# Optimization experiments

Measured on AMD Instinct MI355X. Metric: run time of the kernel, lower is better.

## Reference

```python
import jax, jax.numpy as jnp
import numpy as np

B, J, D, W, H, EH, L = 128, 8192, 32, 4, 128, 256, 32
TEMP = 1.0


def _ln(x, g, b, eps=1e-5):
    mu = jnp.mean(x, axis=-1, keepdims=True)
    var = jnp.var(x, axis=-1, keepdims=True)
    return (x - mu) * jax.lax.rsqrt(var + eps) * g + b


def setup_inputs() -> dict:
    key = jax.random.key(0)
    ks = jax.random.split(key, 12)

    def lin(k, fi, fo):
        k1, k2 = jax.random.split(k)
        s = 1.0 / np.sqrt(fi)
        return (jax.random.uniform(k1, (fi, fo), minval=-s, maxval=s, dtype=jnp.float32),
                jax.random.uniform(k2, (fo,), minval=-s, maxval=s, dtype=jnp.float32))

    h_w1, h_b1 = lin(ks[0], 1 + D, H)
    h_w2, h_b2 = lin(ks[1], H, D)
    g_w1, g_b1 = lin(ks[2], D, D // 2)
    g_w2, g_b2 = lin(ks[3], D // 2, W)
    c_w, c_b = lin(ks[4], W * D, D)
    e_w1, e_b1 = lin(ks[5], D, EH)
    e_w2, e_b2 = lin(ks[6], EH, 2 * L)
    return {
        'x': jax.random.normal(ks[7], (B, J), dtype=jnp.float32),
        'mask': jax.random.randint(ks[8], (B, J), 0, 2, dtype=jnp.int32),
        'fe': jax.random.normal(ks[9], (J, D), dtype=jnp.float32),
        'h_w1': h_w1, 'h_b1': h_b1,
        'h_ln1_w': jnp.ones((H,), jnp.float32), 'h_ln1_b': jnp.zeros((H,), jnp.float32),
        'h_w2': h_w2, 'h_b2': h_b2,
        'h_ln2_w': jnp.ones((D,), jnp.float32), 'h_ln2_b': jnp.zeros((D,), jnp.float32),
        'g_w1': g_w1, 'g_b1': g_b1, 'g_w2': g_w2, 'g_b2': g_b2,
        'c_w': c_w, 'c_b': c_b,
        'c_ln_w': jnp.ones((D,), jnp.float32), 'c_ln_b': jnp.zeros((D,), jnp.float32),
        'e_w1': e_w1, 'e_b1': e_b1,
        'e_ln1_w': jnp.ones((EH,), jnp.float32), 'e_ln1_b': jnp.zeros((EH,), jnp.float32),
        'e_w2': e_w2, 'e_b2': e_b2,
        'e_ln2_w': jnp.ones((2 * L,), jnp.float32), 'e_ln2_b': jnp.zeros((2 * L,), jnp.float32),
    }


def _forward(x, mask, fe, h_w1, h_b1, h_ln1_w, h_ln1_b, h_w2, h_b2, h_ln2_w, h_ln2_b,
             g_w1, g_b1, g_w2, g_b2, c_w, c_b, c_ln_w, c_ln_b,
             e_w1, e_b1, e_ln1_w, e_ln1_b, e_w2, e_b2, e_ln2_w, e_ln2_b):
    relu = jax.nn.relu
    # h_in = concat([x, F]) @ h_w1 split into scalar column + shared embedding part
    # (fe @ h_w1[1:]) is [J,H], shared across cells -> avoids materializing [B,J,1+D]
    pre = x[..., None] * h_w1[0][None, None, :] + (fe @ h_w1[1:])[None] + h_b1  # [B,J,H]
    h1 = relu(_ln(pre, h_ln1_w, h_ln1_b))
    h_out = relu(_ln(h1 @ h_w2 + h_b2, h_ln2_w, h_ln2_b))  # [B,J,D]
    raw_gates = relu(h_out @ g_w1 + g_b1) @ g_w2 + g_b2  # [B,J,W]
    logits = jnp.clip(raw_gates * TEMP, -10.0, 10.0)
    logits = jnp.where(mask[..., None] > 0, logits, -1e9)  # masked gather -> -inf fill
    weights = jax.nn.softmax(logits, axis=1)  # softmax over observed junctions
    head_sums = jnp.einsum('bjw,bjd->bwd', weights, h_out)  # [B,W,D]
    comb = relu(_ln(head_sums.reshape(head_sums.shape[0], -1) @ c_w + c_b, c_ln_w, c_ln_b))
    comb = jnp.where((jnp.sum(mask, axis=1) > 0)[:, None], comb, 0.0)  # zero cells -> zeros
    h = relu(_ln(comb @ e_w1 + e_b1, e_ln1_w, e_ln1_b))
    o = relu(_ln(h @ e_w2 + e_b2, e_ln2_w, e_ln2_b))
    mu, logvar = jnp.split(o, 2, axis=-1)
    return mu, logvar


def reference(x, mask, fe, h_w1, h_b1, h_ln1_w, h_ln1_b, h_w2, h_b2, h_ln2_w, h_ln2_b,
              g_w1, g_b1, g_w2, g_b2, c_w, c_b, c_ln_w, c_ln_b,
              e_w1, e_b1, e_ln1_w, e_ln1_b, e_w2, e_b2, e_ln2_w, e_ln2_b):
    return _forward(x, mask, fe, h_w1, h_b1, h_ln1_w, h_ln1_b, h_w2, h_b2, h_ln2_w, h_ln2_b,
                    g_w1, g_b1, g_w2, g_b2, c_w, c_b, c_ln_w, c_ln_b,
                    e_w1, e_b1, e_ln1_w, e_ln1_b, e_w2, e_b2, e_ln2_w, e_ln2_b)
```

## Files before the change

kernel.cpp:

```cpp
#include <hip/hip_runtime.h>
#include <cstdint>

#define BDIM 128
#define JDIM 8192

typedef short s8x __attribute__((ext_vector_type(8)));
typedef float f4x __attribute__((ext_vector_type(4)));

__device__ __forceinline__ unsigned int rne16(float f) {
    unsigned int u = __float_as_uint(f);
    return (u + 0x7fffu + ((u >> 16) & 1u)) >> 16;
}
__device__ __forceinline__ unsigned int pkbf(float lo, float hi) {
    return rne16(lo) | (rne16(hi) << 16);
}
__device__ __forceinline__ float bf2f(unsigned int s) {
    return __uint_as_float(s << 16);
}

__global__ __launch_bounds__(128) void k_prep(
    const float* __restrict__ fe, const float* __restrict__ hw1,
    const float* __restrict__ hb1,
    unsigned short* __restrict__ feWb, float* __restrict__ aux,
    float* __restrict__ scal)
{
    const int j = blockIdx.x, h = threadIdx.x;
    float acc = hb1[h];
#pragma unroll
    for (int d = 0; d < 32; ++d)
        acc = fmaf(fe[j * 32 + d], hw1[(1 + d) * 128 + h], acc);
    feWb[(size_t)j * 128 + h] = (unsigned short)rne16(acc);

    const float w0h = hw1[h];
    float s1 = acc, sx = w0h * acc, s2 = acc * acc;
#pragma unroll
    for (int m = 1; m <= 32; m <<= 1) {
        s1 += __shfl_xor(s1, m); sx += __shfl_xor(sx, m); s2 += __shfl_xor(s2, m);
    }
    __shared__ float red[2][3];
    const int wv = threadIdx.x >> 6, ln = threadIdx.x & 63;
    if (ln == 0) { red[wv][0] = s1; red[wv][1] = sx; red[wv][2] = s2; }
    __syncthreads();
    if (threadIdx.x == 0) {
        aux[j * 4 + 0] = (red[0][0] + red[1][0]) * (1.f / 128.f);
        aux[j * 4 + 1] = (red[0][1] + red[1][1]) * (1.f / 128.f);
        aux[j * 4 + 2] = (red[0][2] + red[1][2]) * (1.f / 128.f);
    }
    if (j == 0) {
        float a = w0h, b = w0h * w0h;
#pragma unroll
        for (int m = 1; m <= 32; m <<= 1) { a += __shfl_xor(a, m); b += __shfl_xor(b, m); }
        __syncthreads();
        if (ln == 0) { red[wv][0] = a; red[wv][1] = b; }
        __syncthreads();
        if (threadIdx.x == 0) {
            scal[0] = (red[0][0] + red[1][0]) * (1.f / 128.f);
            scal[1] = (red[0][1] + red[1][1]) * (1.f / 128.f);
        }
    }
}

__global__ __launch_bounds__(256, 2) void k_main(
    const float* __restrict__ x, const int* __restrict__ mask,
    const unsigned short* __restrict__ feWb, const float* __restrict__ aux,
    const float* __restrict__ scal,
    const float* __restrict__ hw1, const float* __restrict__ ln1w,
    const float* __restrict__ ln1b,
    const float* __restrict__ hw2, const float* __restrict__ hb2,
    const float* __restrict__ ln2w, const float* __restrict__ ln2b,
    const float* __restrict__ gw1, const float* __restrict__ gb1,
    const float* __restrict__ gw2, const float* __restrict__ gb2,
    float* __restrict__ P, float* __restrict__ SEb)
{
    __shared__ float w0s[128], g1s[128], b1s[128];
    __shared__ float holds[8][576];
    __shared__ float hsL[2048];
    __shared__ float seL[64];

    const int tid = threadIdx.x, wv = tid >> 6, l = tid & 63;
    const int c = l & 15, g = l >> 4;
    const int bt = blockIdx.y, bx = blockIdx.x;
    const int b0 = bt * 16;

    if (tid < 128) { w0s[tid] = hw1[tid]; g1s[tid] = ln1w[tid]; b1s[tid] = ln1b[tid]; }
    __syncthreads();

    const float mw0 = scal[0], q0 = scal[1];

    s8x wf[2][4];
#pragma unroll
    for (int nt = 0; nt < 2; ++nt)
#pragma unroll
        for (int t = 0; t < 4; ++t) {
            const int kb = 32 * t + 8 * g, n = 16 * nt + c;
            uint4 u;
            u.x = pkbf(hw2[(kb + 0) * 32 + n], hw2[(kb + 1) * 32 + n]);
            u.y = pkbf(hw2[(kb + 2) * 32 + n], hw2[(kb + 3) * 32 + n]);
            u.z = pkbf(hw2[(kb + 4) * 32 + n], hw2[(kb + 5) * 32 + n]);
            u.w = pkbf(hw2[(kb + 6) * 32 + n], hw2[(kb + 7) * 32 + n]);
            wf[nt][t] = __builtin_bit_cast(s8x, u);
        }
    s8x g1f;
    {
        uint4 u;
        u.x = pkbf(gw1[(8 * g + 0) * 16 + c], gw1[(8 * g + 1) * 16 + c]);
        u.y = pkbf(gw1[(8 * g + 2) * 16 + c], gw1[(8 * g + 3) * 16 + c]);
        u.z = pkbf(gw1[(8 * g + 4) * 16 + c], gw1[(8 * g + 5) * 16 + c]);
        u.w = pkbf(gw1[(8 * g + 6) * 16 + c], gw1[(8 * g + 7) * 16 + c]);
        g1f = __builtin_bit_cast(s8x, u);
    }
    const float hb2a = hb2[c],      hb2b = hb2[16 + c];
    const float g2a  = ln2w[c],     g2b  = ln2w[16 + c];
    const float z2a  = ln2b[c],     z2b  = ln2b[16 + c];
    const float gb1c = gb1[c];
    float gw2c[4], gb2v[4];
#pragma unroll
    for (int w = 0; w < 4; ++w) { gw2c[w] = gw2[c * 4 + w]; gb2v[w] = gb2[w]; }

    const int j0 = (bx * 4 + wv) * 32;
    const float* xrow = x + (size_t)(b0 + c) * JDIM;
    const int*   mrow = mask + (size_t)(b0 + c) * JDIM;

    float hsacc[4][4][2];
    float seacc[4][4];
#pragma unroll
    for (int r = 0; r < 4; ++r)
#pragma unroll
        for (int w = 0; w < 4; ++w) {
            hsacc[r][w][0] = 0.f; hsacc[r][w][1] = 0.f; seacc[r][w] = 0.f;
        }

    for (int jj = 0; jj < 32; ++jj) {
        const int j = j0 + jj;
        const float xv = xrow[j];
        const int   mv = mrow[j];
        const float m1 = aux[j * 4 + 0], qx = aux[j * 4 + 1], q2 = aux[j * 4 + 2];
        const float mu = fmaf(xv, mw0, m1);
        const float e2 = fmaf(xv * xv, q0, fmaf(2.f * xv, qx, q2));
        const float rs = rsqrtf(e2 - mu * mu + 1e-5f);
        const float nms = -mu * rs;

        f4x ca = {0.f, 0.f, 0.f, 0.f}, cbv = {0.f, 0.f, 0.f, 0.f};
        const unsigned short* fj = feWb + (size_t)j * 128;
#pragma unroll
        for (int t = 0; t < 4; ++t) {
            const int kb = 32 * t + 8 * g;
            const uint4 fw = *(const uint4*)(fj + kb);
            const float pf0 = bf2f(fw.x & 0xffffu), pf1 = bf2f(fw.x >> 16);
            const float pf2 = bf2f(fw.y & 0xffffu), pf3 = bf2f(fw.y >> 16);
            const float pf4 = bf2f(fw.z & 0xffffu), pf5 = bf2f(fw.z >> 16);
            const float pf6 = bf2f(fw.w & 0xffffu), pf7 = bf2f(fw.w >> 16);
            const float4 wa = *(const float4*)&w0s[kb];
            const float4 wb = *(const float4*)&w0s[kb + 4];
            const float4 ga = *(const float4*)&g1s[kb];
            const float4 gbq = *(const float4*)&g1s[kb + 4];
            const float4 ba = *(const float4*)&b1s[kb];
            const float4 bb = *(const float4*)&b1s[kb + 4];
            const float h0 = fmaxf(fmaf(fmaf(fmaf(xv, wa.x, pf0), rs, nms), ga.x,  ba.x), 0.f);
            const float h1 = fmaxf(fmaf(fmaf(fmaf(xv, wa.y, pf1), rs, nms), ga.y,  ba.y), 0.f);
            const float h2 = fmaxf(fmaf(fmaf(fmaf(xv, wa.z, pf2), rs, nms), ga.z,  ba.z), 0.f);
            const float h3 = fmaxf(fmaf(fmaf(fmaf(xv, wa.w, pf3), rs, nms), ga.w,  ba.w), 0.f);
            const float h4 = fmaxf(fmaf(fmaf(fmaf(xv, wb.x, pf4), rs, nms), gbq.x, bb.x), 0.f);
            const float h5 = fmaxf(fmaf(fmaf(fmaf(xv, wb.y, pf5), rs, nms), gbq.y, bb.y), 0.f);
            const float h6 = fmaxf(fmaf(fmaf(fmaf(xv, wb.z, pf6), rs, nms), gbq.z, bb.z), 0.f);
            const float h7 = fmaxf(fmaf(fmaf(fmaf(xv, wb.w, pf7), rs, nms), gbq.w, bb.w), 0.f);
            uint4 u;
            u.x = pkbf(h0, h1); u.y = pkbf(h2, h3); u.z = pkbf(h4, h5); u.w = pkbf(h6, h7);
            const s8x af = __builtin_bit_cast(s8x, u);
            ca  = __builtin_amdgcn_mfma_f32_16x16x32_bf16(af, wf[0][t], ca,  0, 0, 0);
            cbv = __builtin_amdgcn_mfma_f32_16x16x32_bf16(af, wf[1][t], cbv, 0, 0, 0);
        }

        float v0[4], v1[4], sr[4], qr[4];
#pragma unroll
        for (int r = 0; r < 4; ++r) {
            v0[r] = ca[r] + hb2a;
            v1[r] = cbv[r] + hb2b;
            sr[r] = v0[r] + v1[r];
            qr[r] = v0[r] * v0[r] + v1[r] * v1[r];
        }
#pragma unroll
        for (int m = 1; m <= 8; m <<= 1)
#pragma unroll
            for (int r = 0; r < 4; ++r) {
                sr[r] += __shfl_xor(sr[r], m);
                qr[r] += __shfl_xor(qr[r], m);
            }
        float ho0[4], ho1[4];
#pragma unroll
        for (int r = 0; r < 4; ++r) {
            const float m2  = sr[r] * 0.03125f;
            const float rs2 = rsqrtf(fmaf(qr[r], 0.03125f, -m2 * m2) + 1e-5f);
            const float nm2 = -m2 * rs2;
            ho0[r] = fmaxf(fmaf(fmaf(v0[r], rs2, nm2), g2a, z2a), 0.f);
            ho1[r] = fmaxf(fmaf(fmaf(v1[r], rs2, nm2), g2b, z2b), 0.f);
        }

        float* hp = &holds[wv * 2 + (jj & 1)][0];
#pragma unroll
        for (int r = 0; r < 4; ++r) {
            hp[(4 * g + r) * 36 + c]      = ho0[r];
            hp[(4 * g + r) * 36 + 16 + c] = ho1[r];
        }
        asm volatile("s_waitcnt lgkmcnt(0)" ::: "memory");
        const float4 ra  = *(const float4*)&hp[c * 36 + 8 * g];
        const float4 rb2 = *(const float4*)&hp[c * 36 + 8 * g + 4];
        uint4 ua;
        ua.x = pkbf(ra.x, ra.y);  ua.y = pkbf(ra.z, ra.w);
        ua.z = pkbf(rb2.x, rb2.y); ua.w = pkbf(rb2.z, rb2.w);
        const s8x af2 = __builtin_bit_cast(s8x, ua);
        f4x gc = {0.f, 0.f, 0.f, 0.f};
        gc = __builtin_amdgcn_mfma_f32_16x16x32_bf16(af2, g1f, gc, 0, 0, 0);

        float pw[16];
#pragma unroll
        for (int r = 0; r < 4; ++r) {
            const float g1r = fmaxf(gc[r] + gb1c, 0.f);
#pragma unroll
            for (int w = 0; w < 4; ++w) pw[r * 4 + w] = g1r * gw2c[w];
        }
#pragma unroll
        for (int m = 1; m <= 8; m <<= 1)
#pragma unroll
            for (int i = 0; i < 16; ++i) pw[i] += __shfl_xor(pw[i], m);

        int mc[4];
#pragma unroll
        for (int r = 0; r < 4; ++r) mc[r] = __shfl(mv, 20 * g + r);

#pragma unroll
        for (int r = 0; r < 4; ++r)
#pragma unroll
            for (int w = 0; w < 4; ++w) {
                const float lg = fminf(fmaxf(pw[r * 4 + w] + gb2v[w], -10.f), 10.f);
                const float e  = (mc[r] > 0) ? __expf(lg - 10.f) : 0.f;
                seacc[r][w] += e;
                hsacc[r][w][0] = fmaf(e, ho0[r], hsacc[r][w][0]);
                hsacc[r][w][1] = fmaf(e, ho1[r], hsacc[r][w][1]);
            }
    }

    for (int ww = 0; ww < 4; ++ww) {
        __syncthreads();
        if (wv == ww) {
#pragma unroll
            for (int r = 0; r < 4; ++r)
#pragma unroll
                for (int w = 0; w < 4; ++w)
#pragma unroll
                    for (int nt = 0; nt < 2; ++nt) {
                        const int idx = ((4 * g + r) * 4 + w) * 32 + c + 16 * nt;
                        if (ww == 0) hsL[idx] = hsacc[r][w][nt];
                        else         hsL[idx] += hsacc[r][w][nt];
                    }
            if (c == 0) {
#pragma unroll
                for (int r = 0; r < 4; ++r)
#pragma unroll
                    for (int w = 0; w < 4; ++w) {
                        const int si = (4 * g + r) * 4 + w;
                        if (ww == 0) seL[si] = seacc[r][w];
                        else         seL[si] += seacc[r][w];
                    }
            }
        }
    }
    __syncthreads();
    const size_t base = ((size_t)bt * 64 + bx) * 2048;
    for (int i = tid; i < 2048; i += 256) P[base + i] = hsL[i];
    if (tid < 64) SEb[((size_t)bt * 64 + bx) * 64 + tid] = seL[tid];
}

__global__ __launch_bounds__(128) void k_tail(
    const float* __restrict__ P, const float* __restrict__ SEb,
    const float* __restrict__ cw, const float* __restrict__ cbv,
    const float* __restrict__ clnw, const float* __restrict__ clnb,
    const float* __restrict__ ew1, const float* __restrict__ eb1,
    const float* __restrict__ l1w, const float* __restrict__ l1b,
    const float* __restrict__ ew2, const float* __restrict__ eb2,
    const float* __restrict__ l2w, const float* __restrict__ l2b,
    float* __restrict__ out)
{
    const int b = blockIdx.x, t = threadIdx.x;
    const int bt = b >> 4, bi = b & 15;
    __shared__ float hsLs[128], combL[32], hL[256], seW[4], sred[64], red[4];

    const float* Pb = P + (size_t)bt * 64 * 2048 + bi * 128;
    float sacc = 0.f;
#pragma unroll 4
    for (int jc = 0; jc < 64; ++jc) sacc += Pb[(size_t)jc * 2048 + t];

    if (t < 64) {
        const int w = t & 3, sl = t >> 2;
        const float* Sb = SEb + (size_t)bt * 64 * 64 + bi * 4 + w;
        float sp = 0.f;
#pragma unroll
        for (int q = 0; q < 4; ++q) sp += Sb[(size_t)(sl * 4 + q) * 64];
        sred[t] = sp;
    }
    __syncthreads();
    if (t < 4) {
        float v = 0.f;
#pragma unroll
        for (int sl = 0; sl < 16; ++sl) v += sred[sl * 4 + t];
        seW[t] = v;
    }
    __syncthreads();
    const bool has = seW[0] > 0.f;
    hsLs[t] = has ? sacc / seW[t >> 5] : 0.f;
    __syncthreads();

    if (t < 32) {
        float cv = cbv[t];
#pragma unroll 4
        for (int f = 0; f < 128; ++f) cv = fmaf(hsLs[f], cw[f * 32 + t], cv);
        float s = cv, q = cv * cv;
#pragma unroll
        for (int m = 1; m <= 16; m <<= 1) { s += __shfl_xor(s, m); q += __shfl_xor(q, m); }
        const float mu = s * (1.f / 32.f);
        const float rsg = rsqrtf(fmaf(q, 1.f / 32.f, -mu * mu) + 1e-5f);
        const float v = fmaf(fmaf(cv, rsg, -mu * rsg), clnw[t], clnb[t]);
        combL[t] = has ? fmaxf(v, 0.f) : 0.f;
    }
    __syncthreads();

    float h0 = eb1[t], h1v = eb1[t + 128];
#pragma unroll 4
    for (int d = 0; d < 32; ++d) {
        const float cd = combL[d];
        h0  = fmaf(cd, ew1[d * 256 + t], h0);
        h1v = fmaf(cd, ew1[d * 256 + t + 128], h1v);
    }
    {
        float s = h0 + h1v, q = h0 * h0 + h1v * h1v;
#pragma unroll
        for (int m = 1; m <= 32; m <<= 1) { s += __shfl_xor(s, m); q += __shfl_xor(q, m); }
        const int wv = t >> 6, ln = t & 63;
        if (ln == 0) { red[wv * 2] = s; red[wv * 2 + 1] = q; }
    }
    __syncthreads();
    {
        const float S = red[0] + red[2], Q = red[1] + red[3];
        const float mu1 = S * (1.f / 256.f);
        const float rs1 = rsqrtf(fmaf(Q, 1.f / 256.f, -mu1 * mu1) + 1e-5f);
        hL[t]       = fmaxf(fmaf(fmaf(h0,  rs1, -mu1 * rs1), l1w[t],       l1b[t]),       0.f);
        hL[t + 128] = fmaxf(fmaf(fmaf(h1v, rs1, -mu1 * rs1), l1w[t + 128], l1b[t + 128]), 0.f);
    }
    __syncthreads();

    if (t < 64) {
        float ov = eb2[t];
#pragma unroll 4
        for (int m = 0; m < 256; ++m) ov = fmaf(hL[m], ew2[m * 64 + t], ov);
        float s = ov, q = ov * ov;
#pragma unroll
        for (int m = 1; m <= 32; m <<= 1) { s += __shfl_xor(s, m); q += __shfl_xor(q, m); }
        const float mu2 = s * (1.f / 64.f);
        const float rs2 = rsqrtf(fmaf(q, 1.f / 64.f, -mu2 * mu2) + 1e-5f);
        const float o = fmaxf(fmaf(fmaf(ov, rs2, -mu2 * rs2), l2w[t], l2b[t]), 0.f);
        if (t < 32) out[b * 32 + t] = o;
        else        out[4096 + b * 32 + (t - 32)] = o;
    }
}

extern "C" void kernel_launch(void* const* d_in, const int* in_sizes, int n_in,
                              void* d_out, int out_size, void* d_ws, size_t ws_size,
                              hipStream_t stream)
{
    (void)in_sizes; (void)n_in; (void)out_size; (void)ws_size;
    const float* x    = (const float*)d_in[0];
    const int*   mask = (const int*)d_in[1];
    const float* fe   = (const float*)d_in[2];
    const float* hw1  = (const float*)d_in[3];
    const float* hb1  = (const float*)d_in[4];
    const float* ln1w = (const float*)d_in[5];
    const float* ln1b = (const float*)d_in[6];
    const float* hw2  = (const float*)d_in[7];
    const float* hb2  = (const float*)d_in[8];
    const float* ln2w = (const float*)d_in[9];
    const float* ln2b = (const float*)d_in[10];
    const float* gw1  = (const float*)d_in[11];
    const float* gb1  = (const float*)d_in[12];
    const float* gw2  = (const float*)d_in[13];
    const float* gb2  = (const float*)d_in[14];
    const float* cw   = (const float*)d_in[15];
    const float* cbv  = (const float*)d_in[16];
    const float* clnw = (const float*)d_in[17];
    const float* clnb = (const float*)d_in[18];
    const float* ew1  = (const float*)d_in[19];
    const float* eb1  = (const float*)d_in[20];
    const float* l1w  = (const float*)d_in[21];
    const float* l1b  = (const float*)d_in[22];
    const float* ew2  = (const float*)d_in[23];
    const float* eb2  = (const float*)d_in[24];
    const float* l2w  = (const float*)d_in[25];
    const float* l2b  = (const float*)d_in[26];

    char* ws = (char*)d_ws;
    unsigned short* feWb = (unsigned short*)ws;
    float* aux  = (float*)(ws + (2u << 20));
    float* scal = (float*)(ws + (2u << 20) + (128u << 10));
    float* P    = (float*)(ws + (2u << 20) + (128u << 10) + 256u);
    float* SEb  = (float*)(ws + (2u << 20) + (128u << 10) + 256u + 8u * 64u * 2048u * 4u);

    hipLaunchKernelGGL(k_prep, dim3(JDIM), dim3(128), 0, stream,
                       fe, hw1, hb1, feWb, aux, scal);
    hipLaunchKernelGGL(k_main, dim3(64, 8), dim3(256), 0, stream,
                       x, mask, feWb, aux, scal,
                       hw1, ln1w, ln1b, hw2, hb2, ln2w, ln2b,
                       gw1, gb1, gw2, gb2, P, SEb);
    hipLaunchKernelGGL(k_tail, dim3(BDIM), dim3(128), 0, stream,
                       P, SEb, cw, cbv, clnw, clnb,
                       ew1, eb1, l1w, l1b, ew2, eb2, l2w, l2b,
                       (float*)d_out);
}
```

Before: 262.9 us.

## Double j-split blocks, use DPP reductions, ballot mask, and raise occupancy

Splits the junction dimension into twice as many blocks (when workspace allows), so the main kernel launches 1024 blocks instead of 512 and each wave handles 16 junctions. It raises the launch-bounds occupancy hint to 4 blocks per CU. It replaces the shfl_xor butterfly reductions across 16 lanes with DPP row operations, builds the mask bits with a ballot instead of per-row shuffles, and uses exp2 with one FMA and a single float4 load for the aux values. The tail kernel now reduces over the variable number of partial blocks, which costs more partial-sum traffic, and the higher occupancy target may force register spills.

New measurement: 284.7 us. 1.08x slower.

```diff
diff --git a/kernel.cpp b/kernel.cpp
--- a/kernel.cpp
+++ b/kernel.cpp
@@ -16,6 +16,19 @@
 }
 __device__ __forceinline__ float bf2f(unsigned int s) {
     return __uint_as_float(s << 16);
+}
+
+template <int CTRL>
+__device__ __forceinline__ float dppadd(float x) {
+    int y = __builtin_amdgcn_update_dpp(0, __builtin_bit_cast(int, x), CTRL, 0xF, 0xF, true);
+    return x + __builtin_bit_cast(float, y);
+}
+__device__ __forceinline__ float allred16(float x) {
+    x = dppadd<0xB1>(x);
+    x = dppadd<0x4E>(x);
+    x = dppadd<0x141>(x);
+    x = dppadd<0x140>(x);
+    return x;
 }
 
 __global__ __launch_bounds__(128) void k_prep(
@@ -60,7 +73,7 @@
     }
 }
 
-__global__ __launch_bounds__(256, 2) void k_main(
+__global__ __launch_bounds__(256, 4) void k_main(
     const float* __restrict__ x, const int* __restrict__ mask,
     const unsigned short* __restrict__ feWb, const float* __restrict__ aux,
     const float* __restrict__ scal,
@@ -70,14 +83,15 @@
     const float* __restrict__ ln2w, const float* __restrict__ ln2b,
     const float* __restrict__ gw1, const float* __restrict__ gb1,
     const float* __restrict__ gw2, const float* __restrict__ gb2,
-    float* __restrict__ P, float* __restrict__ SEb)
+    float* __restrict__ P, float* __restrict__ SEb, int njb, int jpw)
 {
     __shared__ float w0s[128], g1s[128], b1s[128];
     __shared__ float holds[8][576];
     __shared__ float hsL[2048];
     __shared__ float seL[64];
 
-    const int tid = threadIdx.x, wv = tid >> 6, l = tid & 63;
+    const int tid = threadIdx.x, l = tid & 63;
+    const int wv = __builtin_amdgcn_readfirstlane(tid >> 6);
     const int c = l & 15, g = l >> 4;
     const int bt = blockIdx.y, bx = blockIdx.x;
     const int b0 = bt * 16;
@@ -117,7 +131,7 @@
 #pragma unroll
     for (int w = 0; w < 4; ++w) { gw2c[w] = gw2[c * 4 + w]; gb2v[w] = gb2[w]; }
 
-    const int j0 = (bx * 4 + wv) * 32;
+    const int j0 = (bx * 4 + wv) * jpw;
     const float* xrow = x + (size_t)(b0 + c) * JDIM;
     const int*   mrow = mask + (size_t)(b0 + c) * JDIM;
 
@@ -130,11 +144,12 @@
             hsacc[r][w][0] = 0.f; hsacc[r][w][1] = 0.f; seacc[r][w] = 0.f;
         }
 
-    for (int jj = 0; jj < 32; ++jj) {
+    for (int jj = 0; jj < jpw; ++jj) {
         const int j = j0 + jj;
         const float xv = xrow[j];
         const int   mv = mrow[j];
-        const float m1 = aux[j * 4 + 0], qx = aux[j * 4 + 1], q2 = aux[j * 4 + 2];
+        const float4 au = *(const float4*)(aux + j * 4);
+        const float m1 = au.x, qx = au.y, q2 = au.z;
         const float mu = fmaf(xv, mw0, m1);
         const float e2 = fmaf(xv * xv, q0, fmaf(2.f * xv, qx, q2));
         const float rs = rsqrtf(e2 - mu * mu + 1e-5f);
@@ -180,12 +195,7 @@
             qr[r] = v0[r] * v0[r] + v1[r] * v1[r];
         }
 #pragma unroll
-        for (int m = 1; m <= 8; m <<= 1)
-#pragma unroll
-            for (int r = 0; r < 4; ++r) {
-                sr[r] += __shfl_xor(sr[r], m);
-                qr[r] += __shfl_xor(qr[r], m);
-            }
+        for (int r = 0; r < 4; ++r) { sr[r] = allred16(sr[r]); qr[r] = allred16(qr[r]); }
         float ho0[4], ho1[4];
 #pragma unroll
         for (int r = 0; r < 4; ++r) {
@@ -220,20 +230,20 @@
             for (int w = 0; w < 4; ++w) pw[r * 4 + w] = g1r * gw2c[w];
         }
 #pragma unroll
-        for (int m = 1; m <= 8; m <<= 1)
-#pragma unroll
-            for (int i = 0; i < 16; ++i) pw[i] += __shfl_xor(pw[i], m);
-
-        int mc[4];
-#pragma unroll
-        for (int r = 0; r < 4; ++r) mc[r] = __shfl(mv, 20 * g + r);
+        for (int i = 0; i < 16; ++i) pw[i] = allred16(pw[i]);
+
+        const unsigned bm = (unsigned)__ballot(mv > 0);
+        float fm[4];
+#pragma unroll
+        for (int r = 0; r < 4; ++r) fm[r] = (float)((bm >> (4 * g + r)) & 1u);
 
 #pragma unroll
         for (int r = 0; r < 4; ++r)
 #pragma unroll
             for (int w = 0; w < 4; ++w) {
                 const float lg = fminf(fmaxf(pw[r * 4 + w] + gb2v[w], -10.f), 10.f);
-                const float e  = (mc[r] > 0) ? __expf(lg - 10.f) : 0.f;
+                const float e  = fm[r] * __builtin_amdgcn_exp2f(
+                                     fmaf(lg, 1.44269504089f, -14.4269504089f));
                 seacc[r][w] += e;
                 hsacc[r][w][0] = fmaf(e, ho0[r], hsacc[r][w][0]);
                 hsacc[r][w][1] = fmaf(e, ho1[r], hsacc[r][w][1]);
@@ -266,9 +276,9 @@
         }
     }
     __syncthreads();
-    const size_t base = ((size_t)bt * 64 + bx) * 2048;
+    const size_t base = ((size_t)bt * njb + bx) * 2048;
     for (int i = tid; i < 2048; i += 256) P[base + i] = hsL[i];
-    if (tid < 64) SEb[((size_t)bt * 64 + bx) * 64 + tid] = seL[tid];
+    if (tid < 64) SEb[((size_t)bt * njb + bx) * 64 + tid] = seL[tid];
 }
 
 __global__ __launch_bounds__(128) void k_tail(
@@ -279,23 +289,22 @@
     const float* __restrict__ l1w, const float* __restrict__ l1b,
     const float* __restrict__ ew2, const float* __restrict__ eb2,
     const float* __restrict__ l2w, const float* __restrict__ l2b,
-    float* __restrict__ out)
+    float* __restrict__ out, int njb)
 {
     const int b = blockIdx.x, t = threadIdx.x;
     const int bt = b >> 4, bi = b & 15;
     __shared__ float hsLs[128], combL[32], hL[256], seW[4], sred[64], red[4];
 
-    const float* Pb = P + (size_t)bt * 64 * 2048 + bi * 128;
+    const float* Pb = P + (size_t)bt * njb * 2048 + bi * 128;
     float sacc = 0.f;
 #pragma unroll 4
-    for (int jc = 0; jc < 64; ++jc) sacc += Pb[(size_t)jc * 2048 + t];
+    for (int jc = 0; jc < njb; ++jc) sacc += Pb[(size_t)jc * 2048 + t];
 
     if (t < 64) {
-        const int w = t & 3, sl = t >> 2;
-        const float* Sb = SEb + (size_t)bt * 64 * 64 + bi * 4 + w;
+        const int w = t & 3, part = t >> 2;
         float sp = 0.f;
-#pragma unroll
-        for (int q = 0; q < 4; ++q) sp += Sb[(size_t)(sl * 4 + q) * 64];
+        for (int q = part; q < njb; q += 16)
+            sp += SEb[((size_t)bt * njb + q) * 64 + bi * 4 + w];
         sred[t] = sp;
     }
     __syncthreads();
@@ -367,7 +376,7 @@
                               void* d_out, int out_size, void* d_ws, size_t ws_size,
                               hipStream_t stream)
 {
-    (void)in_sizes; (void)n_in; (void)out_size; (void)ws_size;
+    (void)in_sizes; (void)n_in; (void)out_size;
     const float* x    = (const float*)d_in[0];
     const int*   mask = (const int*)d_in[1];
     const float* fe   = (const float*)d_in[2];
@@ -396,21 +405,29 @@
     const float* l2w  = (const float*)d_in[25];
     const float* l2b  = (const float*)d_in[26];
 
+    const size_t base = (2u << 20) + (128u << 10) + 256u;
+    int NJB = 128;
+    {
+        const size_t need = base + (size_t)8 * 128 * 2048 * 4 + (size_t)8 * 128 * 64 * 4;
+        if (ws_size < need) NJB = 64;
+    }
+    const int JPW = JDIM / (NJB * 4);
+
     char* ws = (char*)d_ws;
     unsigned short* feWb = (unsigned short*)ws;
     float* aux  = (float*)(ws + (2u << 20));
     float* scal = (float*)(ws + (2u << 20) + (128u << 10));
-    float* P    = (float*)(ws + (2u << 20) + (128u << 10) + 256u);
-    float* SEb  = (float*)(ws + (2u << 20) + (128u << 10) + 256u + 8u * 64u * 2048u * 4u);
+    float* P    = (float*)(ws + base);
+    float* SEb  = (float*)(ws + base + (size_t)8 * NJB * 2048 * 4);
 
     hipLaunchKernelGGL(k_prep, dim3(JDIM), dim3(128), 0, stream,
                        fe, hw1, hb1, feWb, aux, scal);
-    hipLaunchKernelGGL(k_main, dim3(64, 8), dim3(256), 0, stream,
+    hipLaunchKernelGGL(k_main, dim3(NJB, 8), dim3(256), 0, stream,
                        x, mask, feWb, aux, scal,
                        hw1, ln1w, ln1b, hw2, hb2, ln2w, ln2b,
-                       gw1, gb1, gw2, gb2, P, SEb);
+                       gw1, gb1, gw2, gb2, P, SEb, NJB, JPW);
     hipLaunchKernelGGL(k_tail, dim3(BDIM), dim3(128), 0, stream,
                        P, SEb, cw, cbv, clnw, clnb,
                        ew1, eb1, l1w, l1b, ew2, eb2, l2w, l2b,
-                       (float*)d_out);
-}
+                       (float*)d_out, NJB);
+}
```
